# Kernel tuning notes

Hardware: AMD Instinct MI355X
Metric: run time of the kernel (lower is better)

Reference implementation:

```python
import jax, jax.numpy as jnp
import numpy as np


def _conv(x, w, pad):
    # NCHW conv, stride 1
    return jax.lax.conv_general_dilated(
        x, w, (1, 1), [(pad, pad), (pad, pad)],
        dimension_numbers=('NCHW', 'OIHW', 'NCHW'))


def _bn_relu(x, s, b, m, v):
    # eval-mode BatchNorm2d (running stats) + ReLU, eps=1e-5
    inv = s / jnp.sqrt(v + 1e-5)
    return jax.nn.relu(x * inv[None, :, None, None] + (b - m * inv)[None, :, None, None])


def _pam(x, qw, qb, kw, kb, vw, vb, gamma):
    B, C, H, W = x.shape
    N = H * W
    q = (_conv(x, qw, 0) + qb[None, :, None, None]).reshape(B, -1, N)  # [B,Cr,N]
    k = (_conv(x, kw, 0) + kb[None, :, None, None]).reshape(B, -1, N)  # [B,Cr,N]
    v = (_conv(x, vw, 0) + vb[None, :, None, None]).reshape(B, C, N)   # [B,C,N]
    energy = jnp.einsum('bcn,bcm->bnm', q, k)          # [B,N,N], query n over keys m
    att = jax.nn.softmax(energy, axis=-1)
    out = jnp.einsum('bcm,bnm->bcn', v, att).reshape(B, C, H, W)
    return gamma * out + x


def _cam(x, gamma):
    B, C, H, W = x.shape
    f = x.reshape(B, C, -1)                            # [B,C,N]
    energy = jnp.einsum('bcn,bdn->bcd', f, f)          # [B,C,C]
    energy_new = jnp.max(energy, axis=-1, keepdims=True) - energy
    att = jax.nn.softmax(energy_new, axis=-1)
    out = jnp.einsum('bcd,bdn->bcn', att, f).reshape(B, C, H, W)
    return gamma * out + x


def _forward(x, w5a, bn5a_s, bn5a_b, bn5a_m, bn5a_v,
             pq_w, pq_b, pk_w, pk_b, pv_w, pv_b, p_gamma,
             w51, bn51_s, bn51_b, bn51_m, bn51_v,
             w5c, bn5c_s, bn5c_b, bn5c_m, bn5c_v, c_gamma,
             w52, bn52_s, bn52_b, bn52_m, bn52_v,
             w8, b8):
    feat1 = _bn_relu(_conv(x, w5a, 1), bn5a_s, bn5a_b, bn5a_m, bn5a_v)
    sa_feat = _pam(feat1, pq_w, pq_b, pk_w, pk_b, pv_w, pv_b, p_gamma)
    sa_conv = _bn_relu(_conv(sa_feat, w51, 1), bn51_s, bn51_b, bn51_m, bn51_v)
    feat2 = _bn_relu(_conv(x, w5c, 1), bn5c_s, bn5c_b, bn5c_m, bn5c_v)
    sc_feat = _cam(feat2, c_gamma)
    sc_conv = _bn_relu(_conv(sc_feat, w52, 1), bn52_s, bn52_b, bn52_m, bn52_v)
    feat_sum = sa_conv + sc_conv
    # conv8 = Dropout2d (identity in eval) -> 1x1 conv -> ReLU
    sasc = jax.nn.relu(_conv(feat_sum, w8, 0) + b8[None, :, None, None])
    return sasc


def setup_inputs() -> dict:
    key = jax.random.key(0)
    ks = iter(jax.random.split(key, 48))
    def rn(shape, scale=0.1):
        return jax.random.normal(next(ks), shape, jnp.float32) * scale
    def bn_params(c):
        s = rn((c,), 0.2) + 1.0
        b = rn((c,), 0.1)
        m = rn((c,), 0.1)
        v = jnp.abs(rn((c,), 0.5)) + 0.5
        return s, b, m, v
    Cin, Ci, Cout = 512, 32, 2
    Cr = max(1, Ci // 8)  # = 4
    inp = {}
    inp['x'] = jax.random.normal(next(ks), (4, Cin, 64, 64), jnp.float32)
    inp['w5a'] = rn((Ci, Cin, 3, 3), 0.05)
    inp['bn5a_s'], inp['bn5a_b'], inp['bn5a_m'], inp['bn5a_v'] = bn_params(Ci)
    inp['pq_w'] = rn((Cr, Ci, 1, 1)); inp['pq_b'] = rn((Cr,), 0.01)
    inp['pk_w'] = rn((Cr, Ci, 1, 1)); inp['pk_b'] = rn((Cr,), 0.01)
    inp['pv_w'] = rn((Ci, Ci, 1, 1)); inp['pv_b'] = rn((Ci,), 0.01)
    inp['p_gamma'] = jnp.full((1,), 0.5, jnp.float32)
    inp['w51'] = rn((Ci, Ci, 3, 3))
    inp['bn51_s'], inp['bn51_b'], inp['bn51_m'], inp['bn51_v'] = bn_params(Ci)
    inp['w5c'] = rn((Ci, Cin, 3, 3), 0.05)
    inp['bn5c_s'], inp['bn5c_b'], inp['bn5c_m'], inp['bn5c_v'] = bn_params(Ci)
    inp['c_gamma'] = jnp.full((1,), 0.5, jnp.float32)
    inp['w52'] = rn((Ci, Ci, 3, 3))
    inp['bn52_s'], inp['bn52_b'], inp['bn52_m'], inp['bn52_v'] = bn_params(Ci)
    inp['w8'] = rn((Cout, Ci, 1, 1)); inp['b8'] = rn((Cout,), 0.01)
    return inp


def reference(x, w5a, bn5a_s, bn5a_b, bn5a_m, bn5a_v,
              pq_w, pq_b, pk_w, pk_b, pv_w, pv_b, p_gamma,
              w51, bn51_s, bn51_b, bn51_m, bn51_v,
              w5c, bn5c_s, bn5c_b, bn5c_m, bn5c_v, c_gamma,
              w52, bn52_s, bn52_b, bn52_m, bn52_v,
              w8, b8):
    return _forward(x, w5a, bn5a_s, bn5a_b, bn5a_m, bn5a_v,
                    pq_w, pq_b, pk_w, pk_b, pv_w, pv_b, p_gamma,
                    w51, bn51_s, bn51_b, bn51_m, bn51_v,
                    w5c, bn5c_s, bn5c_b, bn5c_m, bn5c_v, c_gamma,
                    w52, bn52_s, bn52_b, bn52_m, bn52_v,
                    w8, b8)
```

## Files before the change

kernel.cpp:

```cpp
#include <hip/hip_runtime.h>
#include <hip/hip_bf16.h>


typedef __attribute__((ext_vector_type(8))) short bf16x8;
typedef __attribute__((ext_vector_type(4))) float f32x4;

#define O_WPK   0
#define O_W51P  147456
#define O_W52P  152064
#define O_BNA   156672
#define O_W8    156928
#define O_PQW   157000
#define O_PKW   157132
#define O_PVW   157264
#define O_GAM   158320
#define O_Q     158400
#define O_K     223936
#define O_ENE   453312
#define O_F1T   985792
#define O_F2T   1510080
#define O_V     2034368
#define O_XT    461504
#define O_CP    4922048
#define O_PO    4922048
#define O_PS    3116224
#define O_PE2   9437184
#define O_SAT   9961472
#define O_SCT   10240256

__device__ __forceinline__ unsigned short f2b(float f){
  __hip_bfloat16 h = __float2bfloat16(f);
  return *(unsigned short*)&h;
}

__global__ __launch_bounds__(256) void k_prep_nhwc(
  const float* __restrict__ x,
  const float* w5a, const float* w5c,
  const float* w51, const float* w52,
  const float* s0,const float* b0,const float* m0,const float* v0,
  const float* s1,const float* b1,const float* m1,const float* v1,
  const float* s2,const float* b2,const float* m2,const float* v2,
  const float* s3,const float* b3,const float* m3,const float* v3,
  const float* w8,const float* b8,
  const float* pqw,const float* pqb,const float* pkw,const float* pkb,
  const float* pvw,const float* pvb,const float* pg,const float* cg,
  float* ws)
{
  int bx = blockIdx.x;
  int tid = threadIdx.x;
  __shared__ unsigned short t16[64][65];
  if (bx < 2048){
    int y = bx & 63, ct = (bx >> 6) & 7, b = bx >> 9;
    int r0 = tid >> 4, c0 = (tid & 15) * 4;
    const float* xb = x + ((size_t)(b*512 + ct*64))*4096 + y*64;
    #pragma unroll
    for (int i = 0; i < 4; ++i){
      int row = r0 + i*16;
      float4 v = *(const float4*)(xb + (size_t)row*4096 + c0);
      t16[row][c0+0] = f2b(v.x);
      t16[row][c0+1] = f2b(v.y);
      t16[row][c0+2] = f2b(v.z);
      t16[row][c0+3] = f2b(v.w);
    }
    __syncthreads();
    int pixl = tid >> 2, q = tid & 3;
    unsigned short vs[16];
    #pragma unroll
    for (int j = 0; j < 16; ++j) vs[j] = t16[q*16 + j][pixl];
    unsigned u[8];
    #pragma unroll
    for (int j = 0; j < 8; ++j) u[j] = (unsigned)vs[2*j] | ((unsigned)vs[2*j+1] << 16);
    unsigned short* xt = (unsigned short*)(ws + O_XT);
    int cbl = ct*2 + (q>>1);
    size_t off = (((size_t)(b*16 + cbl)*66 + (y+1))*66 + (pixl+1))*32 + (q&1)*16;
    *(uint4*)(xt + off)     = make_uint4(u[0],u[1],u[2],u[3]);
    *(uint4*)(xt + off + 8) = make_uint4(u[4],u[5],u[6],u[7]);
    return;
  }
  int pbx = bx - 2048;
  if (pbx < 1152){
    int id = pbx*256 + tid;
    int tap = id >> 15;
    int r = id & 32767;
    int cb = r >> 11;
    int r2 = r & 2047;
    int co = r2 >> 5, ci = r2 & 31;
    int cin = cb*32 + ci;
    float v = (co < 32) ? w5a[co*4608 + cin*9 + tap] : w5c[(co-32)*4608 + cin*9 + tap];
    ((unsigned short*)ws)[id] = f2b(v);
    return;
  }
  if (pbx < 1231){
    int id = (pbx-1152)*256 + tid;
    if (id >= 20076) return;
    if (id < 9216){ int tap=id>>10, co=(id>>5)&31, ci=id&31;
      ((unsigned short*)(ws + O_W51P))[id] = f2b(w51[co*288 + ci*9 + tap]); return; }
    id -= 9216;
    if (id < 9216){ int tap=id>>10, co=(id>>5)&31, ci=id&31;
      ((unsigned short*)(ws + O_W52P))[id] = f2b(w52[co*288 + ci*9 + tap]); return; }
    id -= 9216;
    if (id < 256){
      int conv = id>>6, ab = (id>>5)&1, c = id&31;
      const float *S,*Bb,*M,*V;
      if (conv==0){S=s0;Bb=b0;M=m0;V=v0;} else if (conv==1){S=s1;Bb=b1;M=m1;V=v1;}
      else if (conv==2){S=s2;Bb=b2;M=m2;V=v2;} else {S=s3;Bb=b3;M=m3;V=v3;}
      float A = S[c] * rsqrtf(V[c] + 1e-5f);
      ws[O_BNA + conv*64 + ab*32 + c] = ab ? (Bb[c] - M[c]*A) : A;
      return; }
    id -= 256;
    if (id < 64){ ws[O_W8+id] = w8[id]; return; } id -= 64;
    if (id < 2){ ws[O_W8+64+id] = b8[id]; return; } id -= 2;
    if (id < 128){ ws[O_PQW+id] = pqw[id]; return; } id -= 128;
    if (id < 4){ ws[O_PQW+128+id] = pqb[id]; return; } id -= 4;
    if (id < 128){ ws[O_PKW+id] = pkw[id]; return; } id -= 128;
    if (id < 4){ ws[O_PKW+128+id] = pkb[id]; return; } id -= 4;
    if (id < 1024){ ws[O_PVW+id] = pvw[id]; return; } id -= 1024;
    if (id < 32){ ws[O_PVW+1024+id] = pvb[id]; return; } id -= 32;
    ws[O_GAM+id] = id ? cg[0] : pg[0];
    return;
  }
  if (pbx < 1491){
    int i = (pbx-1231)*256 + tid;
    if (i >= 66560) return;
    int part = i & 3; int j = i >> 2;
    int rp = j % 260; int bc = j / 260;
    int py, px;
    if (rp < 66){ py = 0; px = rp; }
    else if (rp < 132){ py = 65; px = rp - 66; }
    else if (rp < 196){ py = rp - 131; px = 0; }
    else { py = rp - 195; px = 65; }
    size_t off = (((size_t)bc*66 + py)*66 + px)*32 + part*8;
    *(uint4*)((unsigned short*)(ws + O_XT) + off) = make_uint4(0,0,0,0);
    return;
  }
  {
    int i = (pbx-1491)*256 + tid;
    if (i >= 8320) return;
    int part = i & 3; int j = i >> 2;
    int arr = j / 1040; int rem = j - arr*1040;
    int b = rem / 260; int rp = rem % 260;
    int py, px;
    if (rp < 66){ py = 0; px = rp; }
    else if (rp < 132){ py = 65; px = rp - 66; }
    else if (rp < 196){ py = rp - 131; px = 0; }
    else { py = rp - 195; px = 65; }
    size_t off = (((size_t)(b*66) + py)*66 + px)*32 + part*8;
    unsigned short* base = (unsigned short*)(ws + (arr ? O_SCT : O_SAT));
    *(uint4*)(base + off) = make_uint4(0,0,0,0);
  }
}

__global__ __launch_bounds__(256) void k_conv_mfma(float* __restrict__ ws){
  int mb = blockIdx.x;
  int ks = blockIdx.y;
  int b = mb >> 7;
  int y = (mb >> 1) & 63;
  int xh = mb & 1;
  __shared__ unsigned short Bs[102*40];
  int tid = threadIdx.x;
  int w = tid >> 6, l = tid & 63;
  f32x4 zero = {0.f,0.f,0.f,0.f};
  f32x4 acc0 = zero, acc1 = zero;
  const unsigned short* wp = (const unsigned short*)ws;
  const unsigned short* xt = (const unsigned short*)(ws + O_XT);
  int arow = w*16 + (l & 15);
  int kq = (l >> 4)*8;
  int dyA = tid/136, remA = tid - dyA*136;
  int t1 = tid + 256;
  int dyB = t1/136, remB = t1 - dyB*136;
  int c0o = dyA*2112 + xh*1024 + remA*8;
  int c1o = dyB*2112 + xh*1024 + remB*8;
  int s0o = (dyA*34 + (remA>>2))*40 + (remA&3)*8;
  int s1o = (dyB*34 + (remB>>2))*40 + (remB&3)*8;
  bool hasB = (tid < 152);
  uint4 rA0, rA1;
  {
    const unsigned short* pb_ = xt + ((size_t)((b*16 + ks*4)*66 + y))*2112;
    rA0 = *(const uint4*)(pb_ + c0o);
    if (hasB) rA1 = *(const uint4*)(pb_ + c1o);
  }
  #pragma unroll 1
  for (int cb4 = 0; cb4 < 4; ++cb4){
    int cb = ks*4 + cb4;
    __syncthreads();
    *(uint4*)&Bs[s0o] = rA0;
    if (hasB) *(uint4*)&Bs[s1o] = rA1;
    __syncthreads();
    if (cb4 < 3){
      const unsigned short* pb_ = xt + ((size_t)((b*16 + cb + 1)*66 + y))*2112;
      rA0 = *(const uint4*)(pb_ + c0o);
      if (hasB) rA1 = *(const uint4*)(pb_ + c1o);
    }
    #pragma unroll
    for (int tap = 0; tap < 9; ++tap){
      int dy = tap/3, dx = tap - dy*3;
      bf16x8 af = *(const bf16x8*)(wp + (size_t)(tap*16 + cb)*2048 + arow*32 + kq);
      bf16x8 bv0 = *(const bf16x8*)&Bs[(dy*34 + (l&15) + dx)*40 + kq];
      bf16x8 bv1 = *(const bf16x8*)&Bs[(dy*34 + 16 + (l&15) + dx)*40 + kq];
      acc0 = __builtin_amdgcn_mfma_f32_16x16x32_bf16(af, bv0, acc0, 0, 0, 0);
      acc1 = __builtin_amdgcn_mfma_f32_16x16x32_bf16(af, bv1, acc1, 0, 0, 0);
    }
  }
  float* cp = ws + O_CP + ((size_t)(ks*4 + b))*262144;
  int co0 = w*16 + (l>>4)*4;
  int pixb = y*64 + xh*32 + (l & 15);
  *(f32x4*)&cp[(size_t)pixb*64 + co0]        = acc0;
  *(f32x4*)&cp[(size_t)(pixb+16)*64 + co0]   = acc1;
}

__global__ __launch_bounds__(256) void k_feat(float* __restrict__ ws){
  int bx = blockIdx.x;
  int tid = threadIdx.x;
  __shared__ float Fl[32][68];
  __shared__ float wqs[4][32], wks[4][32], wvs[32][32];
  int b = bx >> 7, chunk = bx & 127;
  for (int i = tid; i < 1280; i += 256){
    if (i < 128)      ((float*)wqs)[i]     = ws[O_PQW + i];
    else if (i < 256) ((float*)wks)[i-128] = ws[O_PKW + (i-128)];
    else              ((float*)wvs)[i-256] = ws[O_PVW + (i-256)];
  }
  int pix = tid >> 3, cg = tid & 7;
  int pixg = (chunk << 5) + pix;
  const float* cpb = ws + O_CP + (size_t)b*262144 + (size_t)pixg*64 + cg*8;
  f32x4 sa_ = *(const f32x4*)(cpb);
  f32x4 sb_ = *(const f32x4*)(cpb + 4);
  {
    f32x4 t0 = *(const f32x4*)(cpb + 1048576);
    f32x4 t1 = *(const f32x4*)(cpb + 1048576 + 4);
    f32x4 t2 = *(const f32x4*)(cpb + 2097152);
    f32x4 t3 = *(const f32x4*)(cpb + 2097152 + 4);
    f32x4 t4 = *(const f32x4*)(cpb + 3145728);
    f32x4 t5 = *(const f32x4*)(cpb + 3145728 + 4);
    sa_ = (sa_ + t0) + (t2 + t4);
    sb_ = (sb_ + t1) + (t3 + t5);
  }
  int co0 = cg*8;
  int conv = co0 >> 5, cc0 = co0 & 31;
  float v8[8];
  #pragma unroll
  for (int j = 0; j < 8; ++j){
    int c = cc0 + j;
    float A = ws[O_BNA + conv*64 + c], Bb = ws[O_BNA + conv*64 + 32 + c];
    float s = (j < 4) ? sa_[j] : sb_[j-4];
    v8[j] = fmaxf(A*s + Bb, 0.f);
  }
  float* fdst = ws + (conv == 0 ? O_F1T : O_F2T) + ((size_t)(b*4096 + pixg))*32 + cc0;
  *(f32x4*)(fdst)     = (f32x4){v8[0],v8[1],v8[2],v8[3]};
  *(f32x4*)(fdst + 4) = (f32x4){v8[4],v8[5],v8[6],v8[7]};
  *(f32x4*)&Fl[pix][co0]     = (f32x4){v8[0],v8[1],v8[2],v8[3]};
  *(f32x4*)&Fl[pix][co0 + 4] = (f32x4){v8[4],v8[5],v8[6],v8[7]};
  __syncthreads();
  if (tid < 128){
    int part = tid >> 5, pixl = tid & 31;
    int n = (chunk << 5) + pixl;
    float fv[32];
    #pragma unroll
    for (int c = 0; c < 32; ++c) fv[c] = Fl[pixl][c];
    float q = ws[O_PQW+128+part], k = ws[O_PKW+128+part];
    #pragma unroll
    for (int c = 0; c < 32; ++c){ q += wqs[part][c]*fv[c]; k += wks[part][c]*fv[c]; }
    ws[O_Q + (((b<<2)+part)<<12) + n] = q;
    ws[O_K + (((b<<2)+part)<<12) + n] = k;
    unsigned short* vbp = (unsigned short*)(ws + O_V);
    #pragma unroll
    for (int j2 = 0; j2 < 8; ++j2){
      int c2 = part*8 + j2;
      float v = ws[O_PVW+1024+c2];
      #pragma unroll
      for (int c = 0; c < 32; ++c) v += wvs[c2][c]*fv[c];
      vbp[(((b<<5)+c2)<<12) + n] = f2b(v);
    }
  }
  {
    int ce = tid >> 3, d0 = (tid & 7) * 4;
    float a0=0.f, a1=0.f, a2=0.f, a3=0.f;
    #pragma unroll 8
    for (int n = 0; n < 32; ++n){
      float fc = Fl[n][32 + ce];
      float f0 = Fl[n][32 + d0], f1 = Fl[n][32 + d0 + 1];
      float f2 = Fl[n][32 + d0 + 2], f3 = Fl[n][32 + d0 + 3];
      a0 = fmaf(fc, f0, a0); a1 = fmaf(fc, f1, a1);
      a2 = fmaf(fc, f2, a2); a3 = fmaf(fc, f3, a3);
    }
    float* pe = ws + O_PE2 + ((size_t)(b*128 + chunk))*1024 + ce*32 + d0;
    *(f32x4*)pe = (f32x4){a0, a1, a2, a3};
  }
}

__global__ __launch_bounds__(256, 6) void k_pam_flash(float* __restrict__ ws){
  int nt = blockIdx.x;
  int b  = blockIdx.y;
  int ms = blockIdx.z;
  __shared__ float Ks[2][4][4][32];
  __shared__ float Ss[4][32];
  __shared__ float Os[4][32][36];
  int tid = threadIdx.x;
  int w = tid >> 6, l = tid & 63;
  int nn = l & 15, g = l >> 4;
  int n0 = (nt<<5) + nn;
  const float LOG2E = 1.44269504f;
  const float BIAS  = -28.8539008f;
  float q0[4], q1[4];
  #pragma unroll
  for (int cr=0;cr<4;++cr){
    q0[cr] = ws[O_Q + (((b<<2)+cr)<<12) + n0] * LOG2E;
    q1[cr] = ws[O_Q + (((b<<2)+cr)<<12) + n0 + 16] * LOG2E;
  }
  int e0i = l*2, cr_s = e0i >> 5, mm_s = e0i & 31;
  int mbase = ms*1024 + w*256;
  const float* ksrc = ws + O_K + (((b<<2)+cr_s)<<12) + mbase + mm_s;
  const unsigned short* vb = (const unsigned short*)(ws + O_V);
  int mo = g*8;
  const unsigned short* vp0 = vb + (((b<<5) + nn)<<12) + mbase + mo;
  const unsigned short* vp1 = vb + (((b<<5) + 16 + nn)<<12) + mbase + mo;
  f32x4 zero = {0.f,0.f,0.f,0.f};
  f32x4 acc00 = zero, acc01 = zero, acc10 = zero, acc11 = zero;
  float lsum0 = 0.f, lsum1 = 0.f;
  bf16x8 a0A = *(const bf16x8*)(vp0);
  bf16x8 a1A = *(const bf16x8*)(vp1);
  float2 kreg = *(const float2*)(ksrc);
  *(float2*)&Ks[0][w][cr_s][mm_s] = kreg;
  bf16x8 a0B, a1B;
  for (int ch = 0; ch < 8; ++ch){
    int buf = ch & 1;
    if (ch < 7){
      int mn = (ch+1)*32;
      a0B = *(const bf16x8*)(vp0 + mn);
      a1B = *(const bf16x8*)(vp1 + mn);
      kreg = *(const float2*)(ksrc + mn);
    }
    float e0[8], e1[8];
    {
      float4 ka, kb;
      ka = *(const float4*)&Ks[buf][w][0][mo];
      kb = *(const float4*)&Ks[buf][w][0][mo+4];
      e0[0]=fmaf(q0[0],ka.x,BIAS); e0[1]=fmaf(q0[0],ka.y,BIAS); e0[2]=fmaf(q0[0],ka.z,BIAS); e0[3]=fmaf(q0[0],ka.w,BIAS);
      e0[4]=fmaf(q0[0],kb.x,BIAS); e0[5]=fmaf(q0[0],kb.y,BIAS); e0[6]=fmaf(q0[0],kb.z,BIAS); e0[7]=fmaf(q0[0],kb.w,BIAS);
      e1[0]=fmaf(q1[0],ka.x,BIAS); e1[1]=fmaf(q1[0],ka.y,BIAS); e1[2]=fmaf(q1[0],ka.z,BIAS); e1[3]=fmaf(q1[0],ka.w,BIAS);
      e1[4]=fmaf(q1[0],kb.x,BIAS); e1[5]=fmaf(q1[0],kb.y,BIAS); e1[6]=fmaf(q1[0],kb.z,BIAS); e1[7]=fmaf(q1[0],kb.w,BIAS);
#define KACC(CR) \
      ka = *(const float4*)&Ks[buf][w][CR][mo]; \
      kb = *(const float4*)&Ks[buf][w][CR][mo+4]; \
      e0[0]=fmaf(q0[CR],ka.x,e0[0]); e0[1]=fmaf(q0[CR],ka.y,e0[1]); e0[2]=fmaf(q0[CR],ka.z,e0[2]); e0[3]=fmaf(q0[CR],ka.w,e0[3]); \
      e0[4]=fmaf(q0[CR],kb.x,e0[4]); e0[5]=fmaf(q0[CR],kb.y,e0[5]); e0[6]=fmaf(q0[CR],kb.z,e0[6]); e0[7]=fmaf(q0[CR],kb.w,e0[7]); \
      e1[0]=fmaf(q1[CR],ka.x,e1[0]); e1[1]=fmaf(q1[CR],ka.y,e1[1]); e1[2]=fmaf(q1[CR],ka.z,e1[2]); e1[3]=fmaf(q1[CR],ka.w,e1[3]); \
      e1[4]=fmaf(q1[CR],kb.x,e1[4]); e1[5]=fmaf(q1[CR],kb.y,e1[5]); e1[6]=fmaf(q1[CR],kb.z,e1[6]); e1[7]=fmaf(q1[CR],kb.w,e1[7]);
      KACC(1)
      KACC(2)
      KACC(3)
#undef KACC
    }
    union { bf16x8 v; unsigned short u[8]; } pb0, pb1;
    #pragma unroll
    for (int j=0;j<8;j++){ float p = __builtin_amdgcn_exp2f(e0[j]); lsum0 += p; pb0.u[j] = f2b(p); }
    #pragma unroll
    for (int j=0;j<8;j++){ float p = __builtin_amdgcn_exp2f(e1[j]); lsum1 += p; pb1.u[j] = f2b(p); }
    acc00 = __builtin_amdgcn_mfma_f32_16x16x32_bf16(a0A, pb0.v, acc00, 0, 0, 0);
    acc01 = __builtin_amdgcn_mfma_f32_16x16x32_bf16(a1A, pb0.v, acc01, 0, 0, 0);
    acc10 = __builtin_amdgcn_mfma_f32_16x16x32_bf16(a0A, pb1.v, acc10, 0, 0, 0);
    acc11 = __builtin_amdgcn_mfma_f32_16x16x32_bf16(a1A, pb1.v, acc11, 0, 0, 0);
    if (ch < 7){
      int nb = buf ^ 1;
      *(float2*)&Ks[nb][w][cr_s][mm_s] = kreg;
      a0A = a0B; a1A = a1B;
    }
  }
  lsum0 += __shfl_xor(lsum0, 16); lsum0 += __shfl_xor(lsum0, 32);
  lsum1 += __shfl_xor(lsum1, 16); lsum1 += __shfl_xor(lsum1, 32);
  if (l < 16){ Ss[w][l] = lsum0; Ss[w][16+l] = lsum1; }
  #pragma unroll
  for (int r=0;r<4;r++){
    Os[w][nn][g*4 + r]         = acc00[r];
    Os[w][nn][16 + g*4 + r]    = acc01[r];
    Os[w][16+nn][g*4 + r]      = acc10[r];
    Os[w][16+nn][16 + g*4 + r] = acc11[r];
  }
  __syncthreads();
  float* PO = ws + O_PO + (size_t)(ms*4+b)*131072 + nt*1024;
  for (int i = tid; i < 1024; i += 256){
    int nn2 = i >> 5, c = i & 31;
    PO[i] = Os[0][nn2][c] + Os[1][nn2][c] + Os[2][nn2][c] + Os[3][nn2][c];
  }
  if (tid < 32)
    ws[O_PS + (ms*4+b)*4096 + (nt<<5) + tid] = Ss[0][tid]+Ss[1][tid]+Ss[2][tid]+Ss[3][tid];
}

__global__ __launch_bounds__(256) void k_finred(float* __restrict__ ws){
  int bx = blockIdx.x;
  int tid = threadIdx.x;
  if (bx < 512){
    int id = bx*256 + tid;
    int cq = (id & 7) * 4;
    int n  = (id >> 3) & 4095;
    int b  = id >> 15;
    size_t pbase = (size_t)(b*4096 + n)*32 + cq;
    int sbase = b*4096 + n;
    f32x4 O = *(const f32x4*)(ws + O_PO + pbase);
    O = O + *(const f32x4*)(ws + O_PO + 524288 + pbase);
    O = O + *(const f32x4*)(ws + O_PO + 1048576 + pbase);
    O = O + *(const f32x4*)(ws + O_PO + 1572864 + pbase);
    float S = ws[O_PS + sbase] + ws[O_PS + 16384 + sbase]
            + ws[O_PS + 32768 + sbase] + ws[O_PS + 49152 + sbase];
    float gam = ws[O_GAM];
    f32x4 f1 = *(const f32x4*)(ws + O_F1T + (size_t)id*4);
    unsigned short h[4];
    #pragma unroll
    for (int j = 0; j < 4; ++j) h[j] = f2b(gam*(O[j]/S) + f1[j]);
    int y = n >> 6, xx = n & 63;
    unsigned short* sat = (unsigned short*)(ws + O_SAT);
    uint2 u; u.x = (unsigned)h[0] | ((unsigned)h[1] << 16);
             u.y = (unsigned)h[2] | ((unsigned)h[3] << 16);
    *(uint2*)&sat[(((size_t)((b*66 + y+1)*66 + xx+1))<<5) + cq] = u;
    return;
  }
  {
    int id = (bx-512)*256 + tid;
    int b = id >> 10, i = id & 1023;
    const float* pe = ws + O_PE2 + ((size_t)b)*131072 + i;
    float s = 0.f;
    #pragma unroll 8
    for (int chk = 0; chk < 128; ++chk) s += pe[chk*1024];
    ws[O_ENE + id] = s;
  }
}

__global__ __launch_bounds__(256) void k_cam_out(float* __restrict__ ws){
  int blk = blockIdx.x;
  int b = blk >> 5;
  int chunk = blk & 31;
  int tid = threadIdx.x;
  int half = tid >> 7;
  int nl = tid & 127;
  int n = (chunk << 7) + nl;
  __shared__ float att[32][33];
  if (tid < 32){
    int c = tid;
    const float* e = ws + O_ENE + (b<<10) + (c<<5);
    float M = -1e30f, mn = 1e30f;
    #pragma unroll
    for (int d=0;d<32;d++){ M = fmaxf(M, e[d]); mn = fminf(mn, e[d]); }
    float mx2 = M - mn;
    float s = 0.f, ex[32];
    #pragma unroll
    for (int d=0;d<32;d++){ ex[d] = __expf((M - e[d]) - mx2); s += ex[d]; }
    float inv = 1.f/s;
    #pragma unroll
    for (int d=0;d<32;d++) att[c][d] = ex[d]*inv;
  }
  __syncthreads();
  const float* fp = ws + O_F2T + (((size_t)b<<12) + n)*32;
  float fv[32];
  #pragma unroll
  for (int j=0;j<8;j++){
    float4 v = *(const float4*)(fp + j*4);
    fv[j*4]=v.x; fv[j*4+1]=v.y; fv[j*4+2]=v.z; fv[j*4+3]=v.w;
  }
  float g = ws[O_GAM+1];
  int c0 = half*16;
  unsigned u[8];
  #pragma unroll
  for (int cp=0; cp<8; ++cp){
    int ca = c0 + 2*cp, cb = ca + 1;
    float o0 = 0.f, o1 = 0.f;
    #pragma unroll
    for (int d=0;d<32;d++){ o0 += att[ca][d]*fv[d]; o1 += att[cb][d]*fv[d]; }
    float r0 = g*o0 + fv[ca], r1 = g*o1 + fv[cb];
    u[cp] = (unsigned)f2b(r0) | ((unsigned)f2b(r1) << 16);
  }
  int y = n >> 6, xcol = n & 63;
  unsigned short* sct = (unsigned short*)(ws + O_SCT);
  size_t base = ((size_t)((b*66 + y+1)*66 + xcol+1))*32 + c0;
  *(uint4*)(sct + base)     = make_uint4(u[0],u[1],u[2],u[3]);
  *(uint4*)(sct + base + 8) = make_uint4(u[4],u[5],u[6],u[7]);
}

__global__ __launch_bounds__(256) void k_final_mfma(float* __restrict__ ws, float* __restrict__ out){
  int y = blockIdx.x, b = blockIdx.y;
  __shared__ unsigned short Bs[2*3*66*40];
  __shared__ float ep[2][2][2][16];
  int tid = threadIdx.x;
  int w = tid >> 6, l = tid & 63;
  int g = l >> 4, col = l & 15;
  const unsigned short* sat = (const unsigned short*)(ws + O_SAT);
  const unsigned short* sct = (const unsigned short*)(ws + O_SCT);
  for (int i = tid; i < 1584; i += 256){
    int row = i >> 2, part = i & 3;
    int conv = row / 198; int rr = row - conv*198;
    int dy = rr / 66; int pix = rr - dy*66;
    const unsigned short* src = (conv ? sct : sat) + ((size_t)((b*66 + y + dy)*66 + pix))*32 + part*8;
    *(uint4*)&Bs[(size_t)row*40 + part*8] = *(const uint4*)src;
  }
  __syncthreads();
  int cohalf = w & 1, ptbase = (w >> 1) * 2;
  const unsigned short* wp[2] = { (const unsigned short*)(ws + O_W51P), (const unsigned short*)(ws + O_W52P) };
  f32x4 zero = {0.f,0.f,0.f,0.f};
  f32x4 acc[2][2] = {{zero,zero},{zero,zero}};
  for (int dy = 0; dy < 3; ++dy){
    for (int dx = 0; dx < 3; ++dx){
      int tap = dy*3 + dx;
      #pragma unroll
      for (int conv = 0; conv < 2; ++conv){
        bf16x8 af = *(const bf16x8*)(wp[conv] + tap*1024 + (cohalf*16 + col)*32 + g*8);
        #pragma unroll
        for (int pt = 0; pt < 2; ++pt){
          int pix = (ptbase + pt)*16 + col + dx;
          bf16x8 bv = *(const bf16x8*)&Bs[(size_t)((conv*3 + dy)*66 + pix)*40 + g*8];
          acc[conv][pt] = __builtin_amdgcn_mfma_f32_16x16x32_bf16(af, bv, acc[conv][pt], 0, 0, 0);
        }
      }
    }
  }
  float p0[2], p1[2];
  #pragma unroll
  for (int pt = 0; pt < 2; ++pt){
    float s0 = 0.f, s1 = 0.f;
    #pragma unroll
    for (int r = 0; r < 4; ++r){
      int co = cohalf*16 + g*4 + r;
      float A1 = ws[O_BNA + 2*64 + co], B1 = ws[O_BNA + 2*64 + 32 + co];
      float A2 = ws[O_BNA + 3*64 + co], B2 = ws[O_BNA + 3*64 + 32 + co];
      float fs = fmaxf(A1*acc[0][pt][r] + B1, 0.f) + fmaxf(A2*acc[1][pt][r] + B2, 0.f);
      s0 += ws[O_W8 + co]*fs;
      s1 += ws[O_W8 + 32 + co]*fs;
    }
    s0 += __shfl_xor(s0, 16); s0 += __shfl_xor(s0, 32);
    s1 += __shfl_xor(s1, 16); s1 += __shfl_xor(s1, 32);
    p0[pt] = s0; p1[pt] = s1;
  }
  if (cohalf == 0 && l < 16){
    #pragma unroll
    for (int pt = 0; pt < 2; ++pt){ ep[w>>1][pt][0][l] = p0[pt]; ep[w>>1][pt][1][l] = p1[pt]; }
  }
  __syncthreads();
  if (cohalf == 1 && l < 16){
    float b80 = ws[O_W8 + 64], b81 = ws[O_W8 + 65];
    #pragma unroll
    for (int pt = 0; pt < 2; ++pt){
      int pix = y*64 + (w>>1)*32 + pt*16 + l;
      float o0 = p0[pt] + ep[w>>1][pt][0][l] + b80;
      float o1 = p1[pt] + ep[w>>1][pt][1][l] + b81;
      out[((b*2+0)<<12) + pix] = fmaxf(o0, 0.f);
      out[((b*2+1)<<12) + pix] = fmaxf(o1, 0.f);
    }
  }
}

extern "C" void kernel_launch(void* const* d_in, const int* in_sizes, int n_in,
                              void* d_out, int out_size, void* d_ws, size_t ws_size,
                              hipStream_t stream) {
  const float* x    = (const float*)d_in[0];
  float* ws = (float*)d_ws;
  float* out = (float*)d_out;

  k_prep_nhwc<<<3572, 256, 0, stream>>>(
      x,
      (const float*)d_in[1], (const float*)d_in[18],
      (const float*)d_in[13], (const float*)d_in[24],
      (const float*)d_in[2],(const float*)d_in[3],(const float*)d_in[4],(const float*)d_in[5],
      (const float*)d_in[19],(const float*)d_in[20],(const float*)d_in[21],(const float*)d_in[22],
      (const float*)d_in[14],(const float*)d_in[15],(const float*)d_in[16],(const float*)d_in[17],
      (const float*)d_in[25],(const float*)d_in[26],(const float*)d_in[27],(const float*)d_in[28],
      (const float*)d_in[29],(const float*)d_in[30],
      (const float*)d_in[6],(const float*)d_in[7],(const float*)d_in[8],(const float*)d_in[9],
      (const float*)d_in[10],(const float*)d_in[11],(const float*)d_in[12],(const float*)d_in[23],
      ws);
  k_conv_mfma<<<dim3(512,4), 256, 0, stream>>>(ws);
  k_feat<<<512, 256, 0, stream>>>(ws);
  k_pam_flash<<<dim3(128,4,4), 256, 0, stream>>>(ws);
  k_finred<<<528, 256, 0, stream>>>(ws);
  k_cam_out<<<128, 256, 0, stream>>>(ws);
  k_final_mfma<<<dim3(64,4), 256, 0, stream>>>(ws, out);
}
```

Baseline: 101.5 us.

## Double-buffer conv input via direct global-to-LDS loads with swizzled layout

Reworks the first 3x3 conv MFMA kernel so each block covers a full 64-pixel row instead of half a row. That halves the grid and gives each wave four accumulator tiles that reuse the same weight fragment. The input slab is staged with global_load_lds into a double-buffered LDS region, so the next channel block loads while the current one computes. The prep kernel now writes the padded NHWC input with an XOR swizzle to avoid LDS bank conflicts on the unpadded rows. Risks are fewer blocks (lower occupancy and parallelism), a larger LDS footprint, and a layout change that any other reader of the same buffer must also follow.

```diff
diff --git a/kernel.cpp b/kernel.cpp
--- a/kernel.cpp
+++ b/kernel.cpp
@@ -4,6 +4,9 @@
 
 typedef __attribute__((ext_vector_type(8))) short bf16x8;
 typedef __attribute__((ext_vector_type(4))) float f32x4;
+
+#define AS1 __attribute__((address_space(1)))
+#define AS3 __attribute__((address_space(3)))
 
 #define O_WPK   0
 #define O_W51P  147456
@@ -72,9 +75,13 @@
     for (int j = 0; j < 8; ++j) u[j] = (unsigned)vs[2*j] | ((unsigned)vs[2*j+1] << 16);
     unsigned short* xt = (unsigned short*)(ws + O_XT);
     int cbl = ct*2 + (q>>1);
-    size_t off = (((size_t)(b*16 + cbl)*66 + (y+1))*66 + (pixl+1))*32 + (q&1)*16;
-    *(uint4*)(xt + off)     = make_uint4(u[0],u[1],u[2],u[3]);
-    *(uint4*)(xt + off + 8) = make_uint4(u[4],u[5],u[6],u[7]);
+    int pxe = pixl + 1;
+    int sw = (pxe >> 1) & 3;
+    int g0 = (2*(q&1)) ^ sw;
+    int g1 = g0 ^ 1;
+    size_t base = (((size_t)(b*16 + cbl)*66 + (y+1))*66 + pxe)*32;
+    *(uint4*)(xt + base + g0*8) = make_uint4(u[0],u[1],u[2],u[3]);
+    *(uint4*)(xt + base + g1*8) = make_uint4(u[4],u[5],u[6],u[7]);
     return;
   }
   int pbx = bx - 2048;
@@ -153,59 +160,69 @@
 __global__ __launch_bounds__(256) void k_conv_mfma(float* __restrict__ ws){
   int mb = blockIdx.x;
   int ks = blockIdx.y;
-  int b = mb >> 7;
-  int y = (mb >> 1) & 63;
-  int xh = mb & 1;
-  __shared__ unsigned short Bs[102*40];
+  int b = mb >> 6, y = mb & 63;
+  __shared__ __align__(16) unsigned short Bs[2][6336];
   int tid = threadIdx.x;
   int w = tid >> 6, l = tid & 63;
+  int bl = l & 15, qh = l >> 4;
   f32x4 zero = {0.f,0.f,0.f,0.f};
-  f32x4 acc0 = zero, acc1 = zero;
+  f32x4 acc[4] = {zero, zero, zero, zero};
   const unsigned short* wp = (const unsigned short*)ws;
   const unsigned short* xt = (const unsigned short*)(ws + O_XT);
-  int arow = w*16 + (l & 15);
-  int kq = (l >> 4)*8;
-  int dyA = tid/136, remA = tid - dyA*136;
-  int t1 = tid + 256;
-  int dyB = t1/136, remB = t1 - dyB*136;
-  int c0o = dyA*2112 + xh*1024 + remA*8;
-  int c1o = dyB*2112 + xh*1024 + remB*8;
-  int s0o = (dyA*34 + (remA>>2))*40 + (remA&3)*8;
-  int s1o = (dyB*34 + (remB>>2))*40 + (remB&3)*8;
-  bool hasB = (tid < 152);
-  uint4 rA0, rA1;
-  {
-    const unsigned short* pb_ = xt + ((size_t)((b*16 + ks*4)*66 + y))*2112;
-    rA0 = *(const uint4*)(pb_ + c0o);
-    if (hasB) rA1 = *(const uint4*)(pb_ + c1o);
-  }
-  #pragma unroll 1
-  for (int cb4 = 0; cb4 < 4; ++cb4){
-    int cb = ks*4 + cb4;
-    __syncthreads();
-    *(uint4*)&Bs[s0o] = rA0;
-    if (hasB) *(uint4*)&Bs[s1o] = rA1;
-    __syncthreads();
-    if (cb4 < 3){
-      const unsigned short* pb_ = xt + ((size_t)((b*16 + cb + 1)*66 + y))*2112;
-      rA0 = *(const uint4*)(pb_ + c0o);
-      if (hasB) rA1 = *(const uint4*)(pb_ + c1o);
-    }
-    #pragma unroll
-    for (int tap = 0; tap < 9; ++tap){
-      int dy = tap/3, dx = tap - dy*3;
-      bf16x8 af = *(const bf16x8*)(wp + (size_t)(tap*16 + cb)*2048 + arow*32 + kq);
-      bf16x8 bv0 = *(const bf16x8*)&Bs[(dy*34 + (l&15) + dx)*40 + kq];
-      bf16x8 bv1 = *(const bf16x8*)&Bs[(dy*34 + 16 + (l&15) + dx)*40 + kq];
-      acc0 = __builtin_amdgcn_mfma_f32_16x16x32_bf16(af, bv0, acc0, 0, 0, 0);
-      acc1 = __builtin_amdgcn_mfma_f32_16x16x32_bf16(af, bv1, acc1, 0, 0, 0);
-    }
-  }
+  int arow = w*16 + bl;
+  int kq = qh*8;
+  int qx0 = ((qh ^ ((bl>>1)&3)) << 3) + bl*32;
+  int qx1 = ((qh ^ (((bl+1)>>1)&3)) << 3) + (bl+1)*32;
+  int qx2 = ((qh ^ (((bl+2)>>1)&3)) << 3) + (bl+2)*32;
+
+#define CF_STAGE(BUF, CB) { \
+    const unsigned short* slab = xt + (size_t)((b*16 + (CB))*66 + y)*2112; \
+    _Pragma("unroll") \
+    for (int cc = 0; cc < 3; ++cc){ \
+      int kk = w*3 + cc; \
+      __builtin_amdgcn_global_load_lds((const AS1 unsigned int*)(slab + kk*512 + l*8), \
+                                       (AS3 unsigned int*)(&Bs[BUF][kk*512]), 16, 0, 0); \
+    } \
+    if (w == 3 && l < 24) \
+      __builtin_amdgcn_global_load_lds((const AS1 unsigned int*)(slab + 6144 + l*8), \
+                                       (AS3 unsigned int*)(&Bs[BUF][6144]), 16, 0, 0); \
+  }
+
+#define CF_COMPUTE(BUF, CB) { \
+    _Pragma("unroll") \
+    for (int tap = 0; tap < 9; ++tap){ \
+      int dy = tap/3, dx = tap - dy*3; \
+      int qx = (dx==0) ? qx0 : (dx==1) ? qx1 : qx2; \
+      bf16x8 af = *(const bf16x8*)(wp + (size_t)(tap*16 + (CB))*2048 + arow*32 + kq); \
+      _Pragma("unroll") \
+      for (int pt = 0; pt < 4; ++pt){ \
+        bf16x8 bv = *(const bf16x8*)&Bs[BUF][dy*2112 + pt*512 + qx]; \
+        acc[pt] = __builtin_amdgcn_mfma_f32_16x16x32_bf16(af, bv, acc[pt], 0, 0, 0); \
+      } \
+    } }
+
+  CF_STAGE(0, ks*4)
+  __syncthreads();
+  CF_STAGE(1, ks*4+1)
+  CF_COMPUTE(0, ks*4)
+  __syncthreads();
+  CF_STAGE(0, ks*4+2)
+  CF_COMPUTE(1, ks*4+1)
+  __syncthreads();
+  CF_STAGE(1, ks*4+3)
+  CF_COMPUTE(0, ks*4+2)
+  __syncthreads();
+  CF_COMPUTE(1, ks*4+3)
+#undef CF_STAGE
+#undef CF_COMPUTE
+
   float* cp = ws + O_CP + ((size_t)(ks*4 + b))*262144;
-  int co0 = w*16 + (l>>4)*4;
-  int pixb = y*64 + xh*32 + (l & 15);
-  *(f32x4*)&cp[(size_t)pixb*64 + co0]        = acc0;
-  *(f32x4*)&cp[(size_t)(pixb+16)*64 + co0]   = acc1;
+  int co0 = w*16 + qh*4;
+  #pragma unroll
+  for (int pt = 0; pt < 4; ++pt){
+    int pix = y*64 + pt*16 + bl;
+    *(f32x4*)&cp[(size_t)pix*64 + co0] = acc[pt];
+  }
 }
 
 __global__ __launch_bounds__(256) void k_feat(float* __restrict__ ws){
@@ -564,7 +581,7 @@
       (const float*)d_in[6],(const float*)d_in[7],(const float*)d_in[8],(const float*)d_in[9],
       (const float*)d_in[10],(const float*)d_in[11],(const float*)d_in[12],(const float*)d_in[23],
       ws);
-  k_conv_mfma<<<dim3(512,4), 256, 0, stream>>>(ws);
+  k_conv_mfma<<<dim3(256,4), 256, 0, stream>>>(ws);
   k_feat<<<512, 256, 0, stream>>>(ws);
   k_pam_flash<<<dim3(128,4,4), 256, 0, stream>>>(ws);
   k_finred<<<528, 256, 0, stream>>>(ws);
```

Result: faster. 94.96 us (-6.5%).
